# Kernel tuning notes

Measured on AMD Instinct MI355X. Metric: run time of the kernel, lower is better.

## Reference

```python
import jax, jax.numpy as jnp
import numpy as np

C = 1024            # hidden_dim // compression_rate
IN_DIM = 1024
OUT_DIM = 1024
FFT_LEN = C // 2 + 1
CURV = 1e-4         # self.c
EPS = 1e-7
LN_EPS = 1e-5


def _mobius_scalar_mul(r, x, c):
    # r (x) x = tanh(r * atanh(sqrt(c)||x||)) * x / (sqrt(c)||x||)
    sqrt_c = jnp.sqrt(c)
    norm = jnp.maximum(jnp.linalg.norm(x, axis=-1, keepdims=True), EPS)
    scn = jnp.clip(sqrt_c * norm, EPS, 1.0 - 1e-5)
    return jnp.tanh(r * jnp.arctanh(scn)) * x / (sqrt_c * norm)


def _mobius_add(x, y, c):
    x2 = jnp.sum(x * x, axis=-1, keepdims=True)
    y2 = jnp.sum(y * y, axis=-1, keepdims=True)
    xy = jnp.sum(x * y, axis=-1, keepdims=True)
    num = (1.0 + 2.0 * c * xy + c * y2) * x + (1.0 - c * x2) * y
    den = 1.0 + 2.0 * c * xy + (c * c) * x2 * y2
    return num / jnp.maximum(den, EPS)


def _poincare_ball_layer(u, v, c, t):
    # geodesic-style interpolation: ((1-t) (x) u) (+) (t (x) v)
    return _mobius_add(_mobius_scalar_mul(1.0 - t, u, c),
                       _mobius_scalar_mul(t, v, c), c)


def setup_inputs() -> dict:
    key = jax.random.key(0)
    k_x, k_p, k_d = jax.random.split(key, 3)
    std = 0.02
    x = jax.random.normal(k_x, (4, 2048, IN_DIM), dtype=jnp.float32)
    proj_w = jax.random.normal(k_p, (C, IN_DIM), dtype=jnp.float32) * std
    freq_w = jnp.zeros((FFT_LEN,), dtype=jnp.float32)
    t = jnp.float32(0.3)
    ln_g = jnp.ones((C,), dtype=jnp.float32)
    ln_b = jnp.zeros((C,), dtype=jnp.float32)
    down_w = jax.random.normal(k_d, (OUT_DIM, C), dtype=jnp.float32) * std
    scale = jnp.float32(1.0)
    return {"x": x, "proj_w": proj_w, "ln_g": ln_g, "ln_b": ln_b,
            "freq_w": freq_w, "t": t, "down_w": down_w, "scale": scale}


def reference(x, proj_w, ln_g, ln_b, freq_w, t, down_w, scale):
    B, L, _ = x.shape
    # non-sep branch (hidden_dim > in_dim): silu(Linear(x))
    comp = jax.nn.silu(jnp.einsum('bli,ci->blc', x, proj_w))
    mu = jnp.mean(comp, axis=-1, keepdims=True)
    var = jnp.var(comp, axis=-1, keepdims=True)
    comp = (comp - mu) * jax.lax.rsqrt(var + LN_EPS) * ln_g + ln_b
    comp = comp.reshape(-1, C)                     # [B*L, C]
    Xf = jnp.fft.rfft(comp, axis=1)                # [B*L, C//2+1]
    w = jax.nn.softmax(freq_w)[None, :]
    flat = jnp.fft.irfft(Xf * w, n=C, axis=1)
    flat = jnp.nan_to_num(flat)
    shift = jnp.nan_to_num(t * flat)
    hyp = jnp.nan_to_num(_poincare_ball_layer(flat, shift, CURV, t))
    hyp = hyp.reshape(B, L, C)
    return jnp.einsum('blc,oc->blo', hyp, down_w) * scale
```

## Files before the change

### kernel.cpp

```cpp
#include <hip/hip_runtime.h>
#include <math.h>

typedef float f32x4 __attribute__((ext_vector_type(4)));
typedef __bf16 bf16x8 __attribute__((ext_vector_type(8)));
typedef unsigned short u16x8 __attribute__((ext_vector_type(8)));

__device__ __forceinline__ unsigned short f2bf(float f) {
  unsigned u = __float_as_uint(f);
  unsigned r = (u + 0x7fffu + ((u >> 16) & 1u)) >> 16;
  return (unsigned short)r;
}
__device__ __forceinline__ float bf2f(unsigned short h) {
  return __uint_as_float(((unsigned)h) << 16);
}

__device__ __forceinline__ float blk_sum(float v, float* red, int tid) {
  #pragma unroll
  for (int o = 32; o; o >>= 1) v += __shfl_down(v, o);
  __syncthreads();
  if ((tid & 63) == 0) red[tid >> 6] = v;
  __syncthreads();
  return red[0] + red[1] + red[2] + red[3];
}

__global__ __launch_bounds__(256) void k_s(const float* __restrict__ fw,
                                           float* __restrict__ s,
                                           float* __restrict__ pw) {
  __shared__ float wsh[513];
  __shared__ float red[4];
  int tid = threadIdx.x;
  float m = -1e30f;
  for (int i = tid; i < 513; i += 256) m = fmaxf(m, fw[i]);
  #pragma unroll
  for (int o = 32; o; o >>= 1) m = fmaxf(m, __shfl_down(m, o));
  if ((tid & 63) == 0) red[tid >> 6] = m;
  __syncthreads();
  m = fmaxf(fmaxf(red[0], red[1]), fmaxf(red[2], red[3]));
  float sum = 0.f;
  for (int i = tid; i < 513; i += 256) {
    float e = expf(fw[i] - m);
    wsh[i] = e;
    sum += e;
  }
  sum = blk_sum(sum, red, tid);
  float inv = 1.f / sum;

  if (blockIdx.x == 0) {
    for (int i = tid; i < 513; i += 256) {
      float wn = wsh[i] * inv;
      float cf = (i == 0 || i == 512) ? 1.f : 2.f;
      pw[i] = cf * wn * wn * (1.f / 1024.f);
    }
  }

  int gid = blockIdx.x * 256 + tid;
  int d = gid >> 3;
  int chunk = gid & 7;
  float acc = 0.f;
  for (int f = 1 + chunk; f < 512; f += 8) {
    int p = (f * d) & 1023;
    acc += wsh[f] * __cosf(6.283185307179586f * (float)p * (1.f / 1024.f));
  }
  acc += __shfl_xor(acc, 1);
  acc += __shfl_xor(acc, 2);
  acc += __shfl_xor(acc, 4);
  if (chunk == 0) {
    float tot = wsh[0] + ((d & 1) ? -wsh[512] : wsh[512]) + 2.f * acc;
    s[d] = tot * inv * (1.f / 1024.f);
  }
}

__global__ __launch_bounds__(256) void k_prep(const float* __restrict__ x,
                                              const float* __restrict__ pw,
                                              const float* __restrict__ dw,
                                              const float* __restrict__ s,
                                              unsigned short* __restrict__ xb,
                                              unsigned short* __restrict__ pwb,
                                              unsigned short* __restrict__ dwb,
                                              unsigned short* __restrict__ Sb) {
  int b = blockIdx.x;
  int tid = threadIdx.x;
  if (b < 8192) {
    int i = b * 256 + tid;
    float4 v = ((const float4*)x)[i];
    ushort4 o;
    o.x = f2bf(v.x); o.y = f2bf(v.y); o.z = f2bf(v.z); o.w = f2bf(v.w);
    ((ushort4*)xb)[i] = o;
  } else if (b < 9216) {
    int i = (b - 8192) * 256 + tid;
    float4 v = ((const float4*)pw)[i];
    ushort4 o;
    o.x = f2bf(v.x); o.y = f2bf(v.y); o.z = f2bf(v.z); o.w = f2bf(v.w);
    ((ushort4*)pwb)[i] = o;
  } else if (b < 10240) {
    int i = (b - 9216) * 256 + tid;
    float4 v = ((const float4*)dw)[i];
    ushort4 o;
    o.x = f2bf(v.x); o.y = f2bf(v.y); o.z = f2bf(v.z); o.w = f2bf(v.w);
    ((ushort4*)dwb)[i] = o;
  } else {
    int idx = (b - 10240) * 256 + tid;
    int n = idx >> 8;
    int k0 = (idx & 255) * 4;
    ushort4 o;
    o.x = f2bf(s[(k0 + 0 - n) & 1023]);
    o.y = f2bf(s[(k0 + 1 - n) & 1023]);
    o.z = f2bf(s[(k0 + 2 - n) & 1023]);
    o.w = f2bf(s[(k0 + 3 - n) & 1023]);
    ((ushort4*)Sb)[idx] = o;
  }
}

#define GB_BARRIER asm volatile("s_barrier" ::: "memory")
#define GB_WAITV(N) asm volatile("s_waitcnt vmcnt(" #N ")" ::: "memory")

__global__ __launch_bounds__(256, 2) void k_gemm1w2(const unsigned short* __restrict__ xb,
                                                    const unsigned short* __restrict__ pwb,
                                                    const unsigned short* __restrict__ dwb,
                                                    const unsigned short* __restrict__ Sb,
                                                    unsigned short* __restrict__ comp,
                                                    unsigned short* __restrict__ W2) {
  __shared__ __align__(16) unsigned short As[2][128 * 64];
  __shared__ __align__(16) unsigned short Bs[2][128 * 64];
  const int tid = threadIdx.x;
  const int lane = tid & 63;
  const int wave = tid >> 6;
  const int mrow = lane & 15;
  const int kq = lane >> 4;
  const int sw = mrow & 7;
  const int ar = tid >> 3;
  const int ac = (((tid & 7) ^ (ar & 7))) * 8;

  if (blockIdx.x < 512) {
    const int xcd = blockIdx.x & 7;
    const int j = blockIdx.x >> 3;
    const int ntile = j & 7;
    const int bmIdx = xcd + 8 * (j >> 3);
    const int bm = bmIdx * 128;
    const int bn = ntile * 128;
    const int mhalf = (wave & 1) * 64;
    const int nhalf = (wave >> 1) * 64;
    f32x4 acc[4][4] = {};
    const unsigned short* Abase = xb + (size_t)(bm + ar) * 1024 + ac;
    const unsigned short* Bbase = pwb + (size_t)(bn + ar) * 1024 + ac;

#define G1_STAGE(KT, BUF)                                                                     \
    { const int k0_ = (KT) * 64;                                                              \
      _Pragma("unroll")                                                                       \
      for (int r = 0; r < 4; ++r) {                                                           \
        __builtin_amdgcn_global_load_lds(                                                     \
            (const __attribute__((address_space(1))) void*)(Abase + (size_t)(r * 32) * 1024 + k0_), \
            (__attribute__((address_space(3))) void*)((char*)As[BUF] + r * 4096 + wave * 1024), 16, 0, 0); \
        __builtin_amdgcn_global_load_lds(                                                     \
            (const __attribute__((address_space(1))) void*)(Bbase + (size_t)(r * 32) * 1024 + k0_), \
            (__attribute__((address_space(3))) void*)((char*)Bs[BUF] + r * 4096 + wave * 1024), 16, 0, 0); } }

#define G1_COMP(BUF)                                                                          \
    { const char* AsB = (const char*)As[BUF];                                                 \
      const char* BsB = (const char*)Bs[BUF];                                                 \
      _Pragma("unroll")                                                                       \
      for (int kc = 0; kc < 2; ++kc) {                                                        \
        const int chunk = (kc << 2) | kq;                                                     \
        bf16x8 af[4], bfr[4];                                                                 \
        _Pragma("unroll")                                                                     \
        for (int mt = 0; mt < 4; ++mt)                                                        \
          af[mt] = *(const bf16x8*)(AsB + (mhalf + mt * 16 + mrow) * 128 + ((chunk ^ sw) << 4)); \
        _Pragma("unroll")                                                                     \
        for (int nt = 0; nt < 4; ++nt)                                                        \
          bfr[nt] = *(const bf16x8*)(BsB + (nhalf + nt * 16 + mrow) * 128 + ((chunk ^ sw) << 4)); \
        _Pragma("unroll")                                                                     \
        for (int mt = 0; mt < 4; ++mt)                                                        \
          _Pragma("unroll")                                                                   \
          for (int nt = 0; nt < 4; ++nt)                                                      \
            acc[mt][nt] = __builtin_amdgcn_mfma_f32_16x16x32_bf16(af[mt], bfr[nt], acc[mt][nt], 0, 0, 0); } }

    G1_STAGE(0, 0);
    #pragma unroll 1
    for (int kt = 0; kt < 14; kt += 2) {
      G1_STAGE(kt + 1, 1); GB_WAITV(8); GB_BARRIER; G1_COMP(0); GB_BARRIER;
      G1_STAGE(kt + 2, 0); GB_WAITV(8); GB_BARRIER; G1_COMP(1); GB_BARRIER;
    }
    G1_STAGE(15, 1); GB_WAITV(8); GB_BARRIER; G1_COMP(0); GB_BARRIER;
    GB_WAITV(0); GB_BARRIER; G1_COMP(1);

    const int col = bn + nhalf + (lane & 15);
    const int rbase = bm + mhalf + (lane >> 4) * 4;
    #pragma unroll
    for (int mt = 0; mt < 4; ++mt)
      #pragma unroll
      for (int r = 0; r < 4; ++r) {
        const int row = rbase + mt * 16 + r;
        #pragma unroll
        for (int nt = 0; nt < 4; ++nt) {
          float v = acc[mt][nt][r];
          comp[(size_t)row * 1024 + (col + nt * 16)] = f2bf(v / (1.f + expf(-v)));
        }
      }
    return;
  }

  const int wbid = blockIdx.x - 512;
  const int bm = (wbid >> 4) * 64;
  const int bn = (wbid & 15) * 64;
  const int wm = wave & 1;
  const int wn = wave >> 1;
  f32x4 acc[2][2] = {};
  const unsigned short* Abase = dwb + (size_t)(bm + ar) * 1024 + ac;
  const unsigned short* Bbase = Sb + (size_t)(bn + ar) * 1024 + ac;

#define W2_STAGE(KT, BUF)                                                                     \
  { const int k0_ = (KT) * 64;                                                                \
    _Pragma("unroll")                                                                         \
    for (int r = 0; r < 2; ++r) {                                                             \
      __builtin_amdgcn_global_load_lds(                                                       \
          (const __attribute__((address_space(1))) void*)(Abase + (size_t)(r * 32) * 1024 + k0_), \
          (__attribute__((address_space(3))) void*)((char*)As[BUF] + r * 4096 + wave * 1024), 16, 0, 0); \
      __builtin_amdgcn_global_load_lds(                                                       \
          (const __attribute__((address_space(1))) void*)(Bbase + (size_t)(r * 32) * 1024 + k0_), \
          (__attribute__((address_space(3))) void*)((char*)Bs[BUF] + r * 4096 + wave * 1024), 16, 0, 0); } }

#define W2_COMP(BUF)                                                                          \
  { const char* AsB = (const char*)As[BUF];                                                   \
    const char* BsB = (const char*)Bs[BUF];                                                   \
    _Pragma("unroll")                                                                         \
    for (int kc = 0; kc < 2; ++kc) {                                                          \
      const int chunk = (kc << 2) | kq;                                                       \
      bf16x8 af[2], bfr[2];                                                                   \
      _Pragma("unroll")                                                                       \
      for (int mt = 0; mt < 2; ++mt)                                                          \
        af[mt] = *(const bf16x8*)(AsB + (wm * 32 + mt * 16 + mrow) * 128 + ((chunk ^ sw) << 4)); \
      _Pragma("unroll")                                                                       \
      for (int nt = 0; nt < 2; ++nt)                                                          \
        bfr[nt] = *(const bf16x8*)(BsB + (wn * 32 + nt * 16 + mrow) * 128 + ((chunk ^ sw) << 4)); \
      _Pragma("unroll")                                                                       \
      for (int mt = 0; mt < 2; ++mt)                                                          \
        _Pragma("unroll")                                                                     \
        for (int nt = 0; nt < 2; ++nt)                                                        \
          acc[mt][nt] = __builtin_amdgcn_mfma_f32_16x16x32_bf16(af[mt], bfr[nt], acc[mt][nt], 0, 0, 0); } }

  W2_STAGE(0, 0);
  #pragma unroll 1
  for (int kt = 0; kt < 14; kt += 2) {
    W2_STAGE(kt + 1, 1); GB_WAITV(4); GB_BARRIER; W2_COMP(0); GB_BARRIER;
    W2_STAGE(kt + 2, 0); GB_WAITV(4); GB_BARRIER; W2_COMP(1); GB_BARRIER;
  }
  W2_STAGE(15, 1); GB_WAITV(4); GB_BARRIER; W2_COMP(0); GB_BARRIER;
  GB_WAITV(0); GB_BARRIER; W2_COMP(1);

  const int col = bn + wn * 32 + (lane & 15);
  const int rbase = bm + wm * 32 + (lane >> 4) * 4;
  #pragma unroll
  for (int mt = 0; mt < 2; ++mt)
    #pragma unroll
    for (int nt = 0; nt < 2; ++nt)
      #pragma unroll
      for (int r = 0; r < 4; ++r) {
        int row = rbase + mt * 16 + r;
        W2[(size_t)row * 1024 + (col + nt * 16)] = f2bf(acc[mt][nt][r]);
      }
}

#define BFLY2(ZR, ZI, I, J, C, S)                              \
  {                                                            \
    float tr_ = ZR[J] * (C) - ZI[J] * (S);                     \
    float ti_ = ZR[J] * (S) + ZI[J] * (C);                     \
    ZR[J] = ZR[I] - tr_; ZI[J] = ZI[I] - ti_;                  \
    ZR[I] += tr_;        ZI[I] += ti_;                         \
  }

__global__ __launch_bounds__(256) void k_ln(unsigned short* __restrict__ comp,
                                            const float* __restrict__ ln_g,
                                            const float* __restrict__ ln_b,
                                            const float* __restrict__ pw_par,
                                            float* __restrict__ u2) {
  const int tid = threadIdx.x;
  const int lane = tid & 63;
  const int wv = tid >> 6;
  const int rowA = blockIdx.x * 8 + wv * 2;
  const int rowB = rowA + 1;
  const size_t offA = (size_t)rowA * 1024;
  const size_t offB = (size_t)rowB * 1024;
  const int bl = __brev((unsigned)lane) >> 26;
  const int ybase = bl * 16;

  const u16x8* srcA = (const u16x8*)(comp + offA + ybase);
  const u16x8* srcB = (const u16x8*)(comp + offB + ybase);
  u16x8 a0A = srcA[0], a1A = srcA[1];
  u16x8 a0B = srcB[0], a1B = srcB[1];
  float yA[16], yB[16];
  #pragma unroll
  for (int i = 0; i < 8; ++i) {
    yA[i] = bf2f(a0A[i]); yA[8 + i] = bf2f(a1A[i]);
    yB[i] = bf2f(a0B[i]); yB[8 + i] = bf2f(a1B[i]);
  }

  float s1A = 0.f, s1B = 0.f;
  #pragma unroll
  for (int i = 0; i < 16; ++i) { s1A += yA[i]; s1B += yB[i]; }
  #pragma unroll
  for (int o = 32; o; o >>= 1) { s1A += __shfl_xor(s1A, o); s1B += __shfl_xor(s1B, o); }
  const float muA = s1A * (1.f / 1024.f);
  const float muB = s1B * (1.f / 1024.f);
  float s2A = 0.f, s2B = 0.f;
  #pragma unroll
  for (int i = 0; i < 16; ++i) {
    float dA = yA[i] - muA; s2A += dA * dA;
    float dB = yB[i] - muB; s2B += dB * dB;
  }
  #pragma unroll
  for (int o = 32; o; o >>= 1) { s2A += __shfl_xor(s2A, o); s2B += __shfl_xor(s2B, o); }
  const float invA = rsqrtf(s2A * (1.f / 1024.f) + 1e-5f);
  const float invB = rsqrtf(s2B * (1.f / 1024.f) + 1e-5f);

  const float4* gp = (const float4*)(ln_g + ybase);
  const float4* bp = (const float4*)(ln_b + ybase);
  #pragma unroll
  for (int q = 0; q < 4; ++q) {
    float4 g = gp[q], b = bp[q];
    yA[4 * q + 0] = (yA[4 * q + 0] - muA) * invA * g.x + b.x;
    yA[4 * q + 1] = (yA[4 * q + 1] - muA) * invA * g.y + b.y;
    yA[4 * q + 2] = (yA[4 * q + 2] - muA) * invA * g.z + b.z;
    yA[4 * q + 3] = (yA[4 * q + 3] - muA) * invA * g.w + b.w;
    yB[4 * q + 0] = (yB[4 * q + 0] - muB) * invB * g.x + b.x;
    yB[4 * q + 1] = (yB[4 * q + 1] - muB) * invB * g.y + b.y;
    yB[4 * q + 2] = (yB[4 * q + 2] - muB) * invB * g.z + b.z;
    yB[4 * q + 3] = (yB[4 * q + 3] - muB) * invB * g.w + b.w;
  }
  {
    u16x8 o0A, o1A, o0B, o1B;
    #pragma unroll
    for (int i = 0; i < 8; ++i) {
      o0A[i] = f2bf(yA[i]); o1A[i] = f2bf(yA[8 + i]);
      o0B[i] = f2bf(yB[i]); o1B[i] = f2bf(yB[8 + i]);
    }
    u16x8* dstA = (u16x8*)(comp + offA + ybase);
    u16x8* dstB = (u16x8*)(comp + offB + ybase);
    dstA[0] = o0A; dstA[1] = o1A;
    dstB[0] = o0B; dstB[1] = o1B;
  }

  float zrA[8], ziA[8], zrB[8], ziB[8];
  const int cmap[8] = {0, 4, 2, 6, 1, 5, 3, 7};
  #pragma unroll
  for (int r = 0; r < 8; ++r) {
    zrA[r] = yA[2 * cmap[r]]; ziA[r] = yA[2 * cmap[r] + 1];
    zrB[r] = yB[2 * cmap[r]]; ziB[r] = yB[2 * cmap[r] + 1];
  }

  #pragma unroll
  for (int s = 1; s <= 6; ++s) {
    const int half = 1 << (s - 1);
    const int pos = lane & (half - 1);
    const float ang = -3.14159265358979f * (float)pos / (float)half;
    const float c = __cosf(ang), sn = __sinf(ang);
    const bool hi = (lane & half) != 0;
    const float cs = hi ? -c : c;
    const float ss = hi ? -sn : sn;
    float prA[8], piA[8], prB[8], piB[8];
    #pragma unroll
    for (int r = 0; r < 8; ++r) {
      prA[r] = __shfl_xor(zrA[r], half); piA[r] = __shfl_xor(ziA[r], half);
      prB[r] = __shfl_xor(zrB[r], half); piB[r] = __shfl_xor(ziB[r], half);
    }
    #pragma unroll
    for (int r = 0; r < 8; ++r) {
      {
        const float br = hi ? prA[r] : zrA[r];
        const float bi = hi ? piA[r] : ziA[r];
        const float vr = hi ? zrA[r] : prA[r];
        const float vi = hi ? ziA[r] : piA[r];
        zrA[r] = br + cs * vr - ss * vi;
        ziA[r] = bi + cs * vi + ss * vr;
      }
      {
        const float br = hi ? prB[r] : zrB[r];
        const float bi = hi ? piB[r] : ziB[r];
        const float vr = hi ? zrB[r] : prB[r];
        const float vi = hi ? ziB[r] : piB[r];
        zrB[r] = br + cs * vr - ss * vi;
        ziB[r] = bi + cs * vi + ss * vr;
      }
    }
  }
  {
    const float ang = -3.14159265358979f * (float)lane * (1.f / 64.f);
    const float c = __cosf(ang), sn = __sinf(ang);
    BFLY2(zrA, ziA, 0, 1, c, sn); BFLY2(zrA, ziA, 2, 3, c, sn);
    BFLY2(zrA, ziA, 4, 5, c, sn); BFLY2(zrA, ziA, 6, 7, c, sn);
    BFLY2(zrB, ziB, 0, 1, c, sn); BFLY2(zrB, ziB, 2, 3, c, sn);
    BFLY2(zrB, ziB, 4, 5, c, sn); BFLY2(zrB, ziB, 6, 7, c, sn);
  }
  {
    const float a1_ = -3.14159265358979f * (float)lane * (1.f / 128.f);
    const float a2_ = -3.14159265358979f * (float)(64 + lane) * (1.f / 128.f);
    const float ca = __cosf(a1_), sa = __sinf(a1_);
    const float cb = __cosf(a2_), sb = __sinf(a2_);
    BFLY2(zrA, ziA, 0, 2, ca, sa); BFLY2(zrA, ziA, 4, 6, ca, sa);
    BFLY2(zrA, ziA, 1, 3, cb, sb); BFLY2(zrA, ziA, 5, 7, cb, sb);
    BFLY2(zrB, ziB, 0, 2, ca, sa); BFLY2(zrB, ziB, 4, 6, ca, sa);
    BFLY2(zrB, ziB, 1, 3, cb, sb); BFLY2(zrB, ziB, 5, 7, cb, sb);
  }
  {
    const float a1_ = -3.14159265358979f * (float)lane * (1.f / 256.f);
    const float a2_ = -3.14159265358979f * (float)(64 + lane) * (1.f / 256.f);
    const float a3_ = -3.14159265358979f * (float)(128 + lane) * (1.f / 256.f);
    const float a4_ = -3.14159265358979f * (float)(192 + lane) * (1.f / 256.f);
    const float ca = __cosf(a1_), sa = __sinf(a1_);
    const float cb = __cosf(a2_), sb = __sinf(a2_);
    const float cc = __cosf(a3_), sc = __sinf(a3_);
    const float cd = __cosf(a4_), sd = __sinf(a4_);
    BFLY2(zrA, ziA, 0, 4, ca, sa); BFLY2(zrA, ziA, 1, 5, cb, sb);
    BFLY2(zrA, ziA, 2, 6, cc, sc); BFLY2(zrA, ziA, 3, 7, cd, sd);
    BFLY2(zrB, ziB, 0, 4, ca, sa); BFLY2(zrB, ziB, 1, 5, cb, sb);
    BFLY2(zrB, ziB, 2, 6, cc, sc); BFLY2(zrB, ziB, 3, 7, cd, sd);
  }

  const int srcl = (64 - lane) & 63;
  float mrA[8], miA[8], mrB[8], miB[8];
  #pragma unroll
  for (int r = 0; r < 8; ++r) {
    mrA[r] = __shfl(zrA[7 - r], srcl); miA[r] = __shfl(ziA[7 - r], srcl);
    mrB[r] = __shfl(zrB[7 - r], srcl); miB[r] = __shfl(ziB[7 - r], srcl);
  }
  if (lane == 0) {
    #pragma unroll
    for (int r = 0; r < 8; ++r) {
      mrA[r] = zrA[(8 - r) & 7]; miA[r] = ziA[(8 - r) & 7];
      mrB[r] = zrB[(8 - r) & 7]; miB[r] = ziB[(8 - r) & 7];
    }
  }
  float pA = 0.f, pB = 0.f;
  #pragma unroll
  for (int r = 0; r < 8; ++r) {
    const int k = r * 64 + lane;
    const float ang = -3.14159265358979f * (float)k * (1.f / 512.f);
    const float c = __cosf(ang), sn = __sinf(ang);
    const float w = pw_par[k];
    {
      const float er = 0.5f * (zrA[r] + mrA[r]);
      const float ei = 0.5f * (ziA[r] - miA[r]);
      const float orr = 0.5f * (ziA[r] + miA[r]);
      const float oi = -0.5f * (zrA[r] - mrA[r]);
      const float xr = er + orr * c - oi * sn;
      const float xi = ei + orr * sn + oi * c;
      pA += w * (xr * xr + xi * xi);
    }
    {
      const float er = 0.5f * (zrB[r] + mrB[r]);
      const float ei = 0.5f * (ziB[r] - miB[r]);
      const float orr = 0.5f * (ziB[r] + miB[r]);
      const float oi = -0.5f * (zrB[r] - mrB[r]);
      const float xr = er + orr * c - oi * sn;
      const float xi = ei + orr * sn + oi * c;
      pB += w * (xr * xr + xi * xi);
    }
  }
  if (lane == 0) {
    const float w512 = pw_par[512];
    const float xA = zrA[0] - ziA[0];
    const float xB = zrB[0] - ziB[0];
    pA += w512 * xA * xA;
    pB += w512 * xB * xB;
  }
  #pragma unroll
  for (int o = 32; o; o >>= 1) { pA += __shfl_xor(pA, o); pB += __shfl_xor(pB, o); }
  if (lane == 0) { u2[rowA] = pA; u2[rowB] = pB; }
}

__device__ __forceinline__ float gamma_from_u2(float U2, float tv) {
  const float sc = 0.01f;
  const float c = 1e-4f;
  float nrm = sqrtf(U2);
  float nu = fmaxf(nrm, 1e-7f);
  float su = fminf(fmaxf(sc * nu, 1e-7f), 1.f - 1e-5f);
  float Af = tanhf((1.f - tv) * atanhf(su)) / (sc * nu);
  float nvn = fmaxf(fabsf(tv) * nrm, 1e-7f);
  float svv = fminf(fmaxf(sc * nvn, 1e-7f), 1.f - 1e-5f);
  float Bf = tv * tanhf(tv * atanhf(svv)) / (sc * nvn);
  float x2s = Af * Af * U2, y2s = Bf * Bf * U2, xys = Af * Bf * U2;
  float numc = (1.f + 2.f * c * xys + c * y2s) * Af + (1.f - c * x2s) * Bf;
  float den = fmaxf(1.f + 2.f * c * xys + c * c * x2s * y2s, 1e-7f);
  return numc / den;
}

__global__ __launch_bounds__(256, 2) void k_gemm23(const unsigned short* __restrict__ comp,
                                                   const unsigned short* __restrict__ W2,
                                                   const float* __restrict__ u2,
                                                   const float* __restrict__ t_ptr,
                                                   const float* __restrict__ scale_ptr,
                                                   float* __restrict__ out) {
  __shared__ __align__(16) unsigned short As[2][128 * 64];
  __shared__ __align__(16) unsigned short Bs[2][128 * 64];
  __shared__ float gs[128];
  const int tid = threadIdx.x;
  const int lane = tid & 63;
  const int wave = tid >> 6;
  const int xcd = blockIdx.x & 7;
  const int j = blockIdx.x >> 3;
  const int ntile = j & 7;
  const int bmIdx = xcd + 8 * (j >> 3);
  const int bm = bmIdx * 128;
  const int bn = ntile * 128;
  const int mrow = lane & 15;
  const int kq = lane >> 4;
  const int sw = mrow & 7;
  const int mhalf = (wave & 1) * 64;
  const int nhalf = (wave >> 1) * 64;
  const int ar = tid >> 3;
  const int ac = (((tid & 7) ^ (ar & 7))) * 8;
  const unsigned short* Abase = comp + (size_t)(bm + ar) * 1024 + ac;
  const unsigned short* Bbase = W2 + (size_t)(bn + ar) * 1024 + ac;

  if (tid < 128) gs[tid] = gamma_from_u2(u2[bm + tid], t_ptr[0]) * scale_ptr[0];

  f32x4 acc[4][4] = {};

#define G3_STAGE(KT, BUF)                                                                     \
  { const int k0_ = (KT) * 64;                                                                \
    _Pragma("unroll")                                                                         \
    for (int r = 0; r < 4; ++r) {                                                             \
      __builtin_amdgcn_global_load_lds(                                                       \
          (const __attribute__((address_space(1))) void*)(Abase + (size_t)(r * 32) * 1024 + k0_), \
          (__attribute__((address_space(3))) void*)((char*)As[BUF] + r * 4096 + wave * 1024), 16, 0, 0); \
      __builtin_amdgcn_global_load_lds(                                                       \
          (const __attribute__((address_space(1))) void*)(Bbase + (size_t)(r * 32) * 1024 + k0_), \
          (__attribute__((address_space(3))) void*)((char*)Bs[BUF] + r * 4096 + wave * 1024), 16, 0, 0); } }

#define G3_COMP(BUF)                                                                          \
  { const char* AsB = (const char*)As[BUF];                                                   \
    const char* BsB = (const char*)Bs[BUF];                                                   \
    _Pragma("unroll")                                                                         \
    for (int kc = 0; kc < 2; ++kc) {                                                          \
      const int chunk = (kc << 2) | kq;                                                       \
      bf16x8 af[4], bfr[4];                                                                   \
      _Pragma("unroll")                                                                       \
      for (int mt = 0; mt < 4; ++mt)                                                          \
        af[mt] = *(const bf16x8*)(AsB + (mhalf + mt * 16 + mrow) * 128 + ((chunk ^ sw) << 4)); \
      _Pragma("unroll")                                                                       \
      for (int nt = 0; nt < 4; ++nt)                                                          \
        bfr[nt] = *(const bf16x8*)(BsB + (nhalf + nt * 16 + mrow) * 128 + ((chunk ^ sw) << 4)); \
      _Pragma("unroll")                                                                       \
      for (int mt = 0; mt < 4; ++mt)                                                          \
        _Pragma("unroll")                                                                     \
        for (int nt = 0; nt < 4; ++nt)                                                        \
          acc[mt][nt] = __builtin_amdgcn_mfma_f32_16x16x32_bf16(af[mt], bfr[nt], acc[mt][nt], 0, 0, 0); } }

  G3_STAGE(0, 0);
  #pragma unroll 1
  for (int kt = 0; kt < 14; kt += 2) {
    G3_STAGE(kt + 1, 1); GB_WAITV(8); GB_BARRIER; G3_COMP(0); GB_BARRIER;
    G3_STAGE(kt + 2, 0); GB_WAITV(8); GB_BARRIER; G3_COMP(1); GB_BARRIER;
  }
  G3_STAGE(15, 1); GB_WAITV(8); GB_BARRIER; G3_COMP(0); GB_BARRIER;
  GB_WAITV(0); GB_BARRIER; G3_COMP(1);

  const int col = bn + (wave >> 1) * 64 + (lane & 15);
  const int rbase = bm + (wave & 1) * 64 + (lane >> 4) * 4;
  #pragma unroll
  for (int mt = 0; mt < 4; ++mt)
    #pragma unroll
    for (int r = 0; r < 4; ++r) {
      const int row = rbase + mt * 16 + r;
      const float gsc = gs[row - bm];
      #pragma unroll
      for (int nt = 0; nt < 4; ++nt)
        out[(size_t)row * 1024 + (col + nt * 16)] = acc[mt][nt][r] * gsc;
    }
}

extern "C" void kernel_launch(void* const* d_in, const int* in_sizes, int n_in,
                              void* d_out, int out_size, void* d_ws, size_t ws_size,
                              hipStream_t stream) {
  const float* x      = (const float*)d_in[0];
  const float* proj_w = (const float*)d_in[1];
  const float* ln_g   = (const float*)d_in[2];
  const float* ln_b   = (const float*)d_in[3];
  const float* freq_w = (const float*)d_in[4];
  const float* t_p    = (const float*)d_in[5];
  const float* down_w = (const float*)d_in[6];
  const float* scale  = (const float*)d_in[7];

  char* ws = (char*)d_ws;
  unsigned short* xb   = (unsigned short*)ws;
  unsigned short* pwb  = (unsigned short*)(ws + (16u << 20));
  unsigned short* dwb  = (unsigned short*)(ws + (18u << 20));
  unsigned short* comp = (unsigned short*)(ws + (20u << 20));
  unsigned short* Sb   = (unsigned short*)(ws + (36u << 20));
  unsigned short* W2   = (unsigned short*)(ws + (38u << 20));
  float* s_buf         = (float*)(ws + (40u << 20));
  float* pw_par        = (float*)(ws + (40u << 20) + 4096);
  float* u2            = (float*)(ws + (40u << 20) + 8192);

  k_s<<<32, 256, 0, stream>>>(freq_w, s_buf, pw_par);
  k_prep<<<11264, 256, 0, stream>>>(x, proj_w, down_w, s_buf, xb, pwb, dwb, Sb);
  k_gemm1w2<<<768, 256, 0, stream>>>(xb, pwb, dwb, Sb, comp, W2);
  k_ln<<<1024, 256, 0, stream>>>(comp, ln_g, ln_b, pw_par, u2);
  k_gemm23<<<512, 256, 0, stream>>>(comp, W2, u2, t_p, scale, (float*)d_out);
}
```

Baseline: 173.5 us.

## Merge softmax/prep kernels via cooperative grid sync and precompute FFT twiddle table

Combines the softmax/circulant kernel and the bf16 conversion kernel into one cooperative launch with a grid-wide sync, using a grid-stride loop over the former prep blocks. Extra blocks in that launch also precompute FFT twiddle factors into a global table, which k_ln now loads instead of computing sin/cos per stage. This saves one launch and the per-thread trig work, at the cost of a grid barrier, a fixed 1024-block grid and extra global loads and registers in k_ln.

```diff
diff --git a/kernel.cpp b/kernel.cpp
--- a/kernel.cpp
+++ b/kernel.cpp
@@ -1,5 +1,8 @@
 #include <hip/hip_runtime.h>
+#include <hip/hip_cooperative_groups.h>
 #include <math.h>
+
+namespace cg = cooperative_groups;
 
 typedef float f32x4 __attribute__((ext_vector_type(4)));
 typedef __bf16 bf16x8 __attribute__((ext_vector_type(8)));
@@ -23,91 +26,121 @@
   return red[0] + red[1] + red[2] + red[3];
 }
 
-__global__ __launch_bounds__(256) void k_s(const float* __restrict__ fw,
-                                           float* __restrict__ s,
-                                           float* __restrict__ pw) {
+__global__ __launch_bounds__(256, 4) void k_sprep(const float* __restrict__ fw,
+                                                  const float* __restrict__ x,
+                                                  const float* __restrict__ pw,
+                                                  const float* __restrict__ dw,
+                                                  float* __restrict__ s,
+                                                  float* __restrict__ pwp,
+                                                  float2* __restrict__ twtab,
+                                                  unsigned short* __restrict__ xb,
+                                                  unsigned short* __restrict__ pwb,
+                                                  unsigned short* __restrict__ dwb,
+                                                  unsigned short* __restrict__ Sb) {
   __shared__ float wsh[513];
   __shared__ float red[4];
-  int tid = threadIdx.x;
-  float m = -1e30f;
-  for (int i = tid; i < 513; i += 256) m = fmaxf(m, fw[i]);
-  #pragma unroll
-  for (int o = 32; o; o >>= 1) m = fmaxf(m, __shfl_down(m, o));
-  if ((tid & 63) == 0) red[tid >> 6] = m;
-  __syncthreads();
-  m = fmaxf(fmaxf(red[0], red[1]), fmaxf(red[2], red[3]));
-  float sum = 0.f;
-  for (int i = tid; i < 513; i += 256) {
-    float e = expf(fw[i] - m);
-    wsh[i] = e;
-    sum += e;
-  }
-  sum = blk_sum(sum, red, tid);
-  float inv = 1.f / sum;
-
-  if (blockIdx.x == 0) {
+  const int tid = threadIdx.x;
+
+  if (blockIdx.x < 32) {
+    float m = -1e30f;
+    for (int i = tid; i < 513; i += 256) m = fmaxf(m, fw[i]);
+    #pragma unroll
+    for (int o = 32; o; o >>= 1) m = fmaxf(m, __shfl_down(m, o));
+    if ((tid & 63) == 0) red[tid >> 6] = m;
+    __syncthreads();
+    m = fmaxf(fmaxf(red[0], red[1]), fmaxf(red[2], red[3]));
+    float sum = 0.f;
     for (int i = tid; i < 513; i += 256) {
-      float wn = wsh[i] * inv;
-      float cf = (i == 0 || i == 512) ? 1.f : 2.f;
-      pw[i] = cf * wn * wn * (1.f / 1024.f);
-    }
-  }
-
-  int gid = blockIdx.x * 256 + tid;
-  int d = gid >> 3;
-  int chunk = gid & 7;
-  float acc = 0.f;
-  for (int f = 1 + chunk; f < 512; f += 8) {
-    int p = (f * d) & 1023;
-    acc += wsh[f] * __cosf(6.283185307179586f * (float)p * (1.f / 1024.f));
-  }
-  acc += __shfl_xor(acc, 1);
-  acc += __shfl_xor(acc, 2);
-  acc += __shfl_xor(acc, 4);
-  if (chunk == 0) {
-    float tot = wsh[0] + ((d & 1) ? -wsh[512] : wsh[512]) + 2.f * acc;
-    s[d] = tot * inv * (1.f / 1024.f);
-  }
-}
-
-__global__ __launch_bounds__(256) void k_prep(const float* __restrict__ x,
-                                              const float* __restrict__ pw,
-                                              const float* __restrict__ dw,
-                                              const float* __restrict__ s,
-                                              unsigned short* __restrict__ xb,
-                                              unsigned short* __restrict__ pwb,
-                                              unsigned short* __restrict__ dwb,
-                                              unsigned short* __restrict__ Sb) {
-  int b = blockIdx.x;
-  int tid = threadIdx.x;
-  if (b < 8192) {
-    int i = b * 256 + tid;
-    float4 v = ((const float4*)x)[i];
-    ushort4 o;
-    o.x = f2bf(v.x); o.y = f2bf(v.y); o.z = f2bf(v.z); o.w = f2bf(v.w);
-    ((ushort4*)xb)[i] = o;
-  } else if (b < 9216) {
-    int i = (b - 8192) * 256 + tid;
-    float4 v = ((const float4*)pw)[i];
-    ushort4 o;
-    o.x = f2bf(v.x); o.y = f2bf(v.y); o.z = f2bf(v.z); o.w = f2bf(v.w);
-    ((ushort4*)pwb)[i] = o;
-  } else if (b < 10240) {
-    int i = (b - 9216) * 256 + tid;
-    float4 v = ((const float4*)dw)[i];
-    ushort4 o;
-    o.x = f2bf(v.x); o.y = f2bf(v.y); o.z = f2bf(v.z); o.w = f2bf(v.w);
-    ((ushort4*)dwb)[i] = o;
-  } else {
-    int idx = (b - 10240) * 256 + tid;
-    int n = idx >> 8;
-    int k0 = (idx & 255) * 4;
-    ushort4 o;
-    o.x = f2bf(s[(k0 + 0 - n) & 1023]);
-    o.y = f2bf(s[(k0 + 1 - n) & 1023]);
-    o.z = f2bf(s[(k0 + 2 - n) & 1023]);
-    o.w = f2bf(s[(k0 + 3 - n) & 1023]);
-    ((ushort4*)Sb)[idx] = o;
+      float e = expf(fw[i] - m);
+      wsh[i] = e;
+      sum += e;
+    }
+    sum = blk_sum(sum, red, tid);
+    float inv = 1.f / sum;
+
+    if (blockIdx.x == 0) {
+      for (int i = tid; i < 513; i += 256) {
+        float wn = wsh[i] * inv;
+        float cf = (i == 0 || i == 512) ? 1.f : 2.f;
+        pwp[i] = cf * wn * wn * (1.f / 1024.f);
+      }
+    }
+
+    int gid = blockIdx.x * 256 + tid;
+    int d = gid >> 3;
+    int chunk = gid & 7;
+    float acc = 0.f;
+    for (int f = 1 + chunk; f < 512; f += 8) {
+      int p = (f * d) & 1023;
+      acc += wsh[f] * __cosf(6.283185307179586f * (float)p * (1.f / 1024.f));
+    }
+    acc += __shfl_xor(acc, 1);
+    acc += __shfl_xor(acc, 2);
+    acc += __shfl_xor(acc, 4);
+    if (chunk == 0) {
+      float tot = wsh[0] + ((d & 1) ? -wsh[512] : wsh[512]) + 2.f * acc;
+      s[d] = tot * inv * (1.f / 1024.f);
+    }
+  } else if (blockIdx.x < 38) {
+    int t = (int)(blockIdx.x - 32) * 256 + tid;
+    if (t < 1344) {
+      float ang;
+      bool neg = false;
+      if (t < 384) {
+        int st = (t >> 6) + 1, l = t & 63;
+        int half = 1 << (st - 1);
+        int pos = l & (half - 1);
+        ang = -3.14159265358979f * (float)pos / (float)half;
+        neg = (l & half) != 0;
+      } else if (t < 448) {
+        ang = -3.14159265358979f * (float)(t - 384) * (1.f / 64.f);
+      } else if (t < 512) {
+        ang = -3.14159265358979f * (float)(t - 448) * (1.f / 128.f);
+      } else if (t < 576) {
+        ang = -3.14159265358979f * (float)(64 + (t - 512)) * (1.f / 128.f);
+      } else if (t < 832) {
+        ang = -3.14159265358979f * (float)(t - 576) * (1.f / 256.f);
+      } else {
+        ang = -3.14159265358979f * (float)(t - 832) * (1.f / 512.f);
+      }
+      float c = __cosf(ang), sn = __sinf(ang);
+      if (neg) { c = -c; sn = -sn; }
+      twtab[t] = make_float2(c, sn);
+    }
+  }
+  __threadfence();
+  cg::this_grid().sync();
+
+  for (int b = blockIdx.x; b < 11264; b += (int)gridDim.x) {
+    if (b < 8192) {
+      int i = b * 256 + tid;
+      float4 v = ((const float4*)x)[i];
+      ushort4 o;
+      o.x = f2bf(v.x); o.y = f2bf(v.y); o.z = f2bf(v.z); o.w = f2bf(v.w);
+      ((ushort4*)xb)[i] = o;
+    } else if (b < 9216) {
+      int i = (b - 8192) * 256 + tid;
+      float4 v = ((const float4*)pw)[i];
+      ushort4 o;
+      o.x = f2bf(v.x); o.y = f2bf(v.y); o.z = f2bf(v.z); o.w = f2bf(v.w);
+      ((ushort4*)pwb)[i] = o;
+    } else if (b < 10240) {
+      int i = (b - 9216) * 256 + tid;
+      float4 v = ((const float4*)dw)[i];
+      ushort4 o;
+      o.x = f2bf(v.x); o.y = f2bf(v.y); o.z = f2bf(v.z); o.w = f2bf(v.w);
+      ((ushort4*)dwb)[i] = o;
+    } else {
+      int idx = (b - 10240) * 256 + tid;
+      int n = idx >> 8;
+      int k0 = (idx & 255) * 4;
+      ushort4 o;
+      o.x = f2bf(s[(k0 + 0 - n) & 1023]);
+      o.y = f2bf(s[(k0 + 1 - n) & 1023]);
+      o.z = f2bf(s[(k0 + 2 - n) & 1023]);
+      o.w = f2bf(s[(k0 + 3 - n) & 1023]);
+      ((ushort4*)Sb)[idx] = o;
+    }
   }
 }
 
@@ -272,6 +305,7 @@
                                             const float* __restrict__ ln_g,
                                             const float* __restrict__ ln_b,
                                             const float* __restrict__ pw_par,
+                                            const float2* __restrict__ twtab,
                                             float* __restrict__ u2) {
   const int tid = threadIdx.x;
   const int lane = tid & 63;
@@ -287,6 +321,15 @@
   const u16x8* srcB = (const u16x8*)(comp + offB + ybase);
   u16x8 a0A = srcA[0], a1A = srcA[1];
   u16x8 a0B = srcB[0], a1B = srcB[1];
+
+  float2 tws[6];
+  #pragma unroll
+  for (int st = 0; st < 6; ++st) tws[st] = twtab[st * 64 + lane];
+  float2 tw7 = twtab[384 + lane];
+  float2 tw8a = twtab[448 + lane], tw8b = twtab[512 + lane];
+  float2 tw9a = twtab[576 + lane], tw9b = twtab[640 + lane];
+  float2 tw9c = twtab[704 + lane], tw9d = twtab[768 + lane];
+
   float yA[16], yB[16];
   #pragma unroll
   for (int i = 0; i < 8; ++i) {
@@ -350,12 +393,9 @@
   #pragma unroll
   for (int s = 1; s <= 6; ++s) {
     const int half = 1 << (s - 1);
-    const int pos = lane & (half - 1);
-    const float ang = -3.14159265358979f * (float)pos / (float)half;
-    const float c = __cosf(ang), sn = __sinf(ang);
+    const float cs = tws[s - 1].x;
+    const float ss = tws[s - 1].y;
     const bool hi = (lane & half) != 0;
-    const float cs = hi ? -c : c;
-    const float ss = hi ? -sn : sn;
     float prA[8], piA[8], prB[8], piB[8];
     #pragma unroll
     for (int r = 0; r < 8; ++r) {
@@ -383,38 +423,34 @@
     }
   }
   {
-    const float ang = -3.14159265358979f * (float)lane * (1.f / 64.f);
-    const float c = __cosf(ang), sn = __sinf(ang);
+    const float c = tw7.x, sn = tw7.y;
     BFLY2(zrA, ziA, 0, 1, c, sn); BFLY2(zrA, ziA, 2, 3, c, sn);
     BFLY2(zrA, ziA, 4, 5, c, sn); BFLY2(zrA, ziA, 6, 7, c, sn);
     BFLY2(zrB, ziB, 0, 1, c, sn); BFLY2(zrB, ziB, 2, 3, c, sn);
     BFLY2(zrB, ziB, 4, 5, c, sn); BFLY2(zrB, ziB, 6, 7, c, sn);
   }
   {
-    const float a1_ = -3.14159265358979f * (float)lane * (1.f / 128.f);
-    const float a2_ = -3.14159265358979f * (float)(64 + lane) * (1.f / 128.f);
-    const float ca = __cosf(a1_), sa = __sinf(a1_);
-    const float cb = __cosf(a2_), sb = __sinf(a2_);
+    const float ca = tw8a.x, sa = tw8a.y;
+    const float cb = tw8b.x, sb = tw8b.y;
     BFLY2(zrA, ziA, 0, 2, ca, sa); BFLY2(zrA, ziA, 4, 6, ca, sa);
     BFLY2(zrA, ziA, 1, 3, cb, sb); BFLY2(zrA, ziA, 5, 7, cb, sb);
     BFLY2(zrB, ziB, 0, 2, ca, sa); BFLY2(zrB, ziB, 4, 6, ca, sa);
     BFLY2(zrB, ziB, 1, 3, cb, sb); BFLY2(zrB, ziB, 5, 7, cb, sb);
   }
   {
-    const float a1_ = -3.14159265358979f * (float)lane * (1.f / 256.f);
-    const float a2_ = -3.14159265358979f * (float)(64 + lane) * (1.f / 256.f);
-    const float a3_ = -3.14159265358979f * (float)(128 + lane) * (1.f / 256.f);
-    const float a4_ = -3.14159265358979f * (float)(192 + lane) * (1.f / 256.f);
-    const float ca = __cosf(a1_), sa = __sinf(a1_);
-    const float cb = __cosf(a2_), sb = __sinf(a2_);
-    const float cc = __cosf(a3_), sc = __sinf(a3_);
-    const float cd = __cosf(a4_), sd = __sinf(a4_);
+    const float ca = tw9a.x, sa = tw9a.y;
+    const float cb = tw9b.x, sb = tw9b.y;
+    const float cc = tw9c.x, sc = tw9c.y;
+    const float cd = tw9d.x, sd = tw9d.y;
     BFLY2(zrA, ziA, 0, 4, ca, sa); BFLY2(zrA, ziA, 1, 5, cb, sb);
     BFLY2(zrA, ziA, 2, 6, cc, sc); BFLY2(zrA, ziA, 3, 7, cd, sd);
     BFLY2(zrB, ziB, 0, 4, ca, sa); BFLY2(zrB, ziB, 1, 5, cb, sb);
     BFLY2(zrB, ziB, 2, 6, cc, sc); BFLY2(zrB, ziB, 3, 7, cd, sd);
   }
 
+  float2 twu[8];
+  #pragma unroll
+  for (int r = 0; r < 8; ++r) twu[r] = twtab[832 + r * 64 + lane];
   const int srcl = (64 - lane) & 63;
   float mrA[8], miA[8], mrB[8], miB[8];
   #pragma unroll
@@ -433,8 +469,7 @@
   #pragma unroll
   for (int r = 0; r < 8; ++r) {
     const int k = r * 64 + lane;
-    const float ang = -3.14159265358979f * (float)k * (1.f / 512.f);
-    const float c = __cosf(ang), sn = __sinf(ang);
+    const float c = twu[r].x, sn = twu[r].y;
     const float w = pw_par[k];
     {
       const float er = 0.5f * (zrA[r] + mrA[r]);
@@ -590,10 +625,13 @@
   float* s_buf         = (float*)(ws + (40u << 20));
   float* pw_par        = (float*)(ws + (40u << 20) + 4096);
   float* u2            = (float*)(ws + (40u << 20) + 8192);
-
-  k_s<<<32, 256, 0, stream>>>(freq_w, s_buf, pw_par);
-  k_prep<<<11264, 256, 0, stream>>>(x, proj_w, down_w, s_buf, xb, pwb, dwb, Sb);
+  float2* twtab        = (float2*)(ws + (40u << 20) + 8192 + 32768);
+
+  void* args[] = {(void*)&freq_w, (void*)&x, (void*)&proj_w, (void*)&down_w,
+                  (void*)&s_buf, (void*)&pw_par, (void*)&twtab,
+                  (void*)&xb, (void*)&pwb, (void*)&dwb, (void*)&Sb};
+  hipLaunchCooperativeKernel((void*)k_sprep, dim3(1024), dim3(256), args, 0, stream);
   k_gemm1w2<<<768, 256, 0, stream>>>(xb, pwb, dwb, Sb, comp, W2);
-  k_ln<<<1024, 256, 0, stream>>>(comp, ln_g, ln_b, pw_par, u2);
+  k_ln<<<1024, 256, 0, stream>>>(comp, ln_g, ln_b, pw_par, twtab, u2);
   k_gemm23<<<512, 256, 0, stream>>>(comp, W2, u2, t_p, scale, (float*)d_out);
 }
```

Result: slower. 368.0 us (+112.1%).
